# Kernel tuning notes

Hardware: AMD Instinct MI355X
Metric: run time of the kernel (lower is better)

The kernel has to match this reference:

```python
import jax, jax.numpy as jnp
import numpy as np

B, S, D, H = 2, 2048, 768, 12
DK = D // H


def setup_inputs() -> dict:
    key = jax.random.key(0)
    ks = jax.random.split(key, 10)
    sc = 0.02
    return {
        "k": jax.random.normal(ks[0], (B, S, D), jnp.float32),
        "q": jax.random.normal(ks[1], (B, S, D), jnp.float32),
        "v": jax.random.normal(ks[2], (B, S, D), jnp.float32),
        "mask": jnp.ones((B, 1, S, S), jnp.int32),
        "wq": jax.random.normal(ks[3], (D, D), jnp.float32) * sc,
        "bq": jnp.zeros((D,), jnp.float32),
        "wk": jax.random.normal(ks[4], (D, D), jnp.float32) * sc,
        "bk": jnp.zeros((D,), jnp.float32),
        "wv": jax.random.normal(ks[5], (D, D), jnp.float32) * sc,
        "bv": jnp.zeros((D,), jnp.float32),
        "wo": jax.random.normal(ks[6], (D, D), jnp.float32) * sc,
        "bo": jnp.zeros((D,), jnp.float32),
    }


def reference(k, q, v, mask, wq, bq, wk, bk, wv, bv, wo, bo):
    # Linear projections (torch Linear: x @ W^T + b)
    query = q @ wq.T + bq
    key_ = k @ wk.T + bk
    value = v @ wv.T + bv
    # [B,S,D] -> [B,H,S,DK]
    def split_heads(x):
        return x.reshape(B, S, H, DK).transpose(0, 2, 1, 3)
    Q, K, V = split_heads(query), split_heads(key_), split_heads(value)
    # NOTE: original masked_fill result is discarded -> mask is a no-op.
    scores = jnp.einsum("bhqd,bhkd->bhqk", Q, K) / jnp.sqrt(jnp.float32(DK))
    attn = jax.nn.softmax(scores, axis=-1)  # dropout p=0.0 -> identity
    out = jnp.einsum("bhqk,bhkd->bhqd", attn, V)
    out = out.transpose(0, 2, 1, 3).reshape(B, S, D)
    return out @ wo.T + bo
```

## Files before the change

### kernel.cpp

```cpp
#include <hip/hip_runtime.h>
#include <hip/hip_bf16.h>

#define B_  2
#define S_  2048
#define D_  768
#define H_  12
#define DK_ 64
#define NX_ (B_*S_*D_)
#define NW_ (D_*D_)
#define CSC 0.18033688011112042f

typedef __attribute__((ext_vector_type(8))) short  bf16x8;
typedef __attribute__((ext_vector_type(4))) float  f32x4;

__device__ __forceinline__ unsigned short f2bf(float f) {
    unsigned int u = __float_as_uint(f);
    u += 0x7fffu + ((u >> 16) & 1u);
    return (unsigned short)(u >> 16);
}

__device__ __forceinline__ unsigned pack_bf2(float a, float b) {
    const unsigned ua = __float_as_uint(a) + 0x8000u;
    const unsigned ub = __float_as_uint(b) + 0x8000u;
    return __builtin_amdgcn_perm(ub, ua, 0x07060302u);
}

__device__ __forceinline__ void async_cp16(const unsigned short* g,
                                           const unsigned short* lds_uniform_base) {
    __builtin_amdgcn_global_load_lds(
        (const __attribute__((address_space(1))) unsigned int*)(uintptr_t)g,
        (__attribute__((address_space(3))) unsigned int*)(unsigned int)(uintptr_t)lds_uniform_base,
        16, 0, 0);
}

struct CvtArgs { const float* s[7]; };

__global__ __launch_bounds__(256) void cvt_all(CvtArgs a,
                                               unsigned short* __restrict__ Xsw,
                                               unsigned short* __restrict__ Wsw) {
    const int bx = blockIdx.x;
    int y, inner;
    if (bx < 4608) { y = bx / 1536;       inner = bx % 1536; }
    else           { y = 3 + (bx - 4608) / 288; inner = (bx - 4608) % 288; }
    const int idx = inner * 256 + threadIdx.x;
    const int n = idx / 96;
    const int g = idx % 96;
    const float* src = a.s[y];
    const float zs = (y == 3) ? CSC : 1.0f;
    const float4 f0 = *(const float4*)(src + (long)n * D_ + g * 8);
    const float4 f1 = *(const float4*)(src + (long)n * D_ + g * 8 + 4);
    unsigned short o[8] = {f2bf(f0.x*zs), f2bf(f0.y*zs), f2bf(f0.z*zs), f2bf(f0.w*zs),
                           f2bf(f1.x*zs), f2bf(f1.y*zs), f2bf(f1.z*zs), f2bf(f1.w*zs)};
    const int kdst = (g >> 3) * 64 + (((g & 7) ^ (n & 7)) * 8);
    unsigned short* dst = (y >= 3) ? (Wsw + (long)(y - 3) * NW_) : (Xsw + (long)y * NX_);
    *(uint4*)(dst + (long)n * D_ + kdst) = *(const uint4*)o;
}

struct QkvArgs { const float* bias[3]; unsigned short* out[3]; };

__global__ __launch_bounds__(256, 2) void gemm_qkv(QkvArgs args,
                                                   const unsigned short* __restrict__ Xsw,
                                                   const unsigned short* __restrict__ Wsw) {
    __shared__ __align__(16) unsigned short smem[17408];
    unsigned short* As = smem;
    unsigned short* Bs = smem + 8192;

    const int t    = threadIdx.x;
    const int wave = t >> 6;
    const int lane = t & 63;
    const int l16  = lane & 15;
    const int quad = lane >> 4;
    const int wm   = wave >> 1, wn = wave & 1;
    const int m0   = blockIdx.x * 128;
    const int zz   = blockIdx.y / 6;
    const int nb   = blockIdx.y % 6;
    const int n0   = nb * 128;

    const unsigned short* Ap = Xsw + (long)zz * NX_;
    const unsigned short* Wp = Wsw + (long)zz * NW_;

    f32x4 acc[4][4];
#pragma unroll
    for (int s = 0; s < 4; s++)
#pragma unroll
        for (int j = 0; j < 4; j++) acc[s][j] = (f32x4){0.f, 0.f, 0.f, 0.f};

    const int lrow = lane >> 3;
    const int lcg  = lane & 7;

    for (int k0 = 0; k0 < D_; k0 += 64) {
        __syncthreads();
#pragma unroll
        for (int i = 0; i < 4; i++) {
            const int chunk = wave * 4 + i;
            async_cp16(Ap + (long)(m0 + chunk * 8 + lrow) * D_ + k0 + lcg * 8,
                       As + chunk * 512);
        }
#pragma unroll
        for (int i = 0; i < 4; i++) {
            const int chunk = wave * 4 + i;
            async_cp16(Wp + (long)(n0 + chunk * 8 + lrow) * D_ + k0 + lcg * 8,
                       Bs + chunk * 512);
        }
        __syncthreads();
#pragma unroll
        for (int ks = 0; ks < 2; ks++) {
            const int cg = ks * 4 + quad;
            bf16x8 af[4], bf[4];
#pragma unroll
            for (int s = 0; s < 4; s++) {
                const int r = wm * 64 + s * 16 + l16;
                af[s] = *(const bf16x8*)&As[r * 64 + ((cg ^ (r & 7)) * 8)];
            }
#pragma unroll
            for (int j = 0; j < 4; j++) {
                const int r = wn * 64 + j * 16 + l16;
                bf[j] = *(const bf16x8*)&Bs[r * 64 + ((cg ^ (r & 7)) * 8)];
            }
#pragma unroll
            for (int s = 0; s < 4; s++)
#pragma unroll
                for (int j = 0; j < 4; j++)
                    acc[s][j] = __builtin_amdgcn_mfma_f32_16x16x32_bf16(af[s], bf[j], acc[s][j], 0, 0, 0);
        }
    }
    __syncthreads();

    const int b     = m0 >> 11;
    const int sbase = m0 & (S_ - 1);
    const float zs  = (zz == 0) ? CSC : 1.0f;
    float bv[4];
#pragma unroll
    for (int j = 0; j < 4; j++) bv[j] = args.bias[zz][n0 + wn * 64 + j * 16 + l16] * zs;

    if (zz < 2) {
        unsigned short* Ls = smem;
#pragma unroll
        for (int s = 0; s < 4; s++)
#pragma unroll
            for (int j = 0; j < 4; j++)
#pragma unroll
                for (int r = 0; r < 4; r++)
                    Ls[(wm * 64 + s * 16 + quad * 4 + r) * 136 + wn * 64 + j * 16 + l16] =
                        f2bf(acc[s][j][r] + bv[j]);
        __syncthreads();
        const int row  = t >> 1;
        const int half = t & 1;
        unsigned short* Op = args.out[zz];
#pragma unroll
        for (int i = 0; i < 8; i++) {
            const int col  = half * 64 + i * 8;
            const int head = nb * 2 + half;
            const uint4 v = *(const uint4*)&Ls[row * 136 + col];
            *(uint4*)(Op + ((long)(b * H_ + head) * S_ + sbase + row) * DK_ + (col & 63)) = v;
        }
    } else {
        unsigned short* Ls = smem;
#pragma unroll
        for (int s = 0; s < 4; s++)
#pragma unroll
            for (int j = 0; j < 4; j++)
#pragma unroll
                for (int r = 0; r < 4; r++) {
                    const int dk  = j * 16 + l16;
                    const int pos = wm * 64 + (quad * 4 + r) * 4 + s;
                    Ls[wn * 8704 + dk * 136 + pos] = f2bf(acc[s][j][r] + bv[j]);
                }
        __syncthreads();
        const int rowIdx = t >> 1;
        const int hh = rowIdx >> 6, dk = rowIdx & 63;
        const int half = t & 1;
        unsigned short* Op = args.out[2];
#pragma unroll
        for (int i = 0; i < 8; i++) {
            const int col = half * 64 + i * 8;
            const uint4 v = *(const uint4*)&Ls[hh * 8704 + dk * 136 + col];
            const int head = nb * 2 + hh;
            *(uint4*)(Op + ((long)(b * H_ + head) * DK_ + dk) * S_ + sbase + col) = v;
        }
    }
}

__global__ __launch_bounds__(256, 3) void attn_kernel(
    const unsigned short* __restrict__ Q, const unsigned short* __restrict__ K,
    const unsigned short* __restrict__ Vt, unsigned short* __restrict__ Ao)
{
    const int t    = threadIdx.x;
    const int wave = t >> 6;
    const int lane = t & 63;
    const int l16  = lane & 15;
    const int quad = lane >> 4;
    const int qtile = blockIdx.x;
    const int bh    = blockIdx.y;

    const unsigned short* Qp = Q  + (long)bh * S_ * DK_;
    const unsigned short* Kp = K  + (long)bh * S_ * DK_;
    const unsigned short* Vp = Vt + (long)bh * DK_ * S_;

    __shared__ __align__(16) unsigned short smem[23040];

    bf16x8 qfrag[2];
    {
        const long qoff = (long)(qtile * 64 + wave * 16 + l16) * DK_ + quad * 8;
        qfrag[0] = *(const bf16x8*)(Qp + qoff);
        qfrag[1] = *(const bf16x8*)(Qp + qoff + 32);
    }
    unsigned short* Ps = smem + 18432;

    const int srow = t >> 2;
    const int scg  = (t & 3) * 16;
    uint4 kreg[2], vreg[2];
    {
        const unsigned short* gk = Kp + (long)srow * DK_ + scg;
        const unsigned short* gv = Vp + (long)srow * S_ + scg;
        kreg[0] = *(const uint4*)gk;  kreg[1] = *(const uint4*)(gk + 8);
        vreg[0] = *(const uint4*)gv;  vreg[1] = *(const uint4*)(gv + 8);
    }
    *(uint4*)&smem[srow * 72 + scg]            = kreg[0];
    *(uint4*)&smem[srow * 72 + scg + 8]        = kreg[1];
    *(uint4*)&smem[9216 + srow * 72 + scg]     = vreg[0];
    *(uint4*)&smem[9216 + srow * 72 + scg + 8] = vreg[1];

    f32x4 oacc[4];
#pragma unroll
    for (int j = 0; j < 4; j++) oacc[j] = (f32x4){0.f, 0.f, 0.f, 0.f};
    float lsum[4] = {0.f, 0.f, 0.f, 0.f};

    for (int it = 0; it < 32; ++it) {
        const int co = (it & 1) * 4608;
        const int no = ((it & 1) ^ 1) * 4608;
        __syncthreads();
        const unsigned short* Ks = smem + co;
        const unsigned short* Vs = smem + 9216 + co;

        if (it < 31) {
            const int kv0 = (it + 1) * 64;
            const unsigned short* gk = Kp + (long)(kv0 + srow) * DK_ + scg;
            const unsigned short* gv = Vp + (long)srow * S_ + kv0 + scg;
            kreg[0] = *(const uint4*)gk;  kreg[1] = *(const uint4*)(gk + 8);
            vreg[0] = *(const uint4*)gv;  vreg[1] = *(const uint4*)(gv + 8);
        }

        f32x4 sacc[4];
#pragma unroll
        for (int j = 0; j < 4; j++) sacc[j] = (f32x4){0.f, 0.f, 0.f, 0.f};
#pragma unroll
        for (int ks = 0; ks < 2; ks++)
#pragma unroll
            for (int j = 0; j < 4; j++) {
                const bf16x8 bf = *(const bf16x8*)&Ks[(j * 16 + l16) * 72 + ks * 32 + quad * 8];
                sacc[j] = __builtin_amdgcn_mfma_f32_16x16x32_bf16(qfrag[ks], bf, sacc[j], 0, 0, 0);
            }

#pragma unroll
        for (int r = 0; r < 4; r++) {
            const float p0 = exp2f(sacc[0][r]);
            const float p1 = exp2f(sacc[1][r]);
            const float p2 = exp2f(sacc[2][r]);
            const float p3 = exp2f(sacc[3][r]);
            lsum[r] += (p0 + p1) + (p2 + p3);
            uint2 pk = {pack_bf2(p0, p1), pack_bf2(p2, p3)};
            *(uint2*)&Ps[(wave * 16 + quad * 4 + r) * 72 + l16 * 4] = pk;
        }

#pragma unroll
        for (int ks = 0; ks < 2; ks++) {
            const bf16x8 pf = *(const bf16x8*)&Ps[(wave * 16 + l16) * 72 + ks * 32 + quad * 8];
#pragma unroll
            for (int j = 0; j < 4; j++) {
                const bf16x8 vf = *(const bf16x8*)&Vs[(j * 16 + l16) * 72 + ks * 32 + quad * 8];
                oacc[j] = __builtin_amdgcn_mfma_f32_16x16x32_bf16(pf, vf, oacc[j], 0, 0, 0);
            }
        }

        if (it < 31) {
            *(uint4*)&smem[no + srow * 72 + scg]            = kreg[0];
            *(uint4*)&smem[no + srow * 72 + scg + 8]        = kreg[1];
            *(uint4*)&smem[9216 + no + srow * 72 + scg]     = vreg[0];
            *(uint4*)&smem[9216 + no + srow * 72 + scg + 8] = vreg[1];
        }
    }

#pragma unroll
    for (int r = 0; r < 4; r++) {
#pragma unroll
        for (int off = 1; off < 16; off <<= 1)
            lsum[r] += __shfl_xor(lsum[r], off, 64);
        lsum[r] = 1.f / lsum[r];
    }

    __syncthreads();
#pragma unroll
    for (int j = 0; j < 4; j++)
#pragma unroll
        for (int r = 0; r < 4; r++)
            Ps[(wave * 16 + quad * 4 + r) * 72 + j * 16 + l16] =
                f2bf(oacc[j][r] * lsum[r]);

    const int b = bh / H_, h = bh % H_;
    const int row = t >> 2;
    const int c0  = (t & 3) * 16;
    const int qrow = qtile * 64 + row;
    const int key  = qrow & 7;
    const uint4 v0 = *(const uint4*)&Ps[row * 72 + c0];
    const uint4 v1 = *(const uint4*)&Ps[row * 72 + c0 + 8];
    const int g8 = c0 >> 3;
    unsigned short* dst = Ao + (long)(b * S_ + qrow) * D_ + h * DK_;
    *(uint4*)(dst + ((g8 ^ key) * 8))       = v0;
    *(uint4*)(dst + (((g8 + 1) ^ key) * 8)) = v1;
}

__global__ __launch_bounds__(256, 2) void gemm_out(
    const unsigned short* __restrict__ A, const unsigned short* __restrict__ Wsw,
    const float* __restrict__ bias, float* __restrict__ Out)
{
    __shared__ __align__(16) unsigned short smem[17408];
    unsigned short* As = smem;
    unsigned short* Bs = smem + 8192;

    const int t    = threadIdx.x;
    const int wave = t >> 6;
    const int lane = t & 63;
    const int l16  = lane & 15;
    const int quad = lane >> 4;
    const int wm   = wave >> 1, wn = wave & 1;
    const int m0   = blockIdx.x * 128;
    const int n0   = blockIdx.y * 128;

    f32x4 acc[4][4];
#pragma unroll
    for (int s = 0; s < 4; s++)
#pragma unroll
        for (int j = 0; j < 4; j++) acc[s][j] = (f32x4){0.f, 0.f, 0.f, 0.f};

    const int lrow = lane >> 3;
    const int lcg  = lane & 7;

    for (int k0 = 0; k0 < D_; k0 += 64) {
        __syncthreads();
#pragma unroll
        for (int i = 0; i < 4; i++) {
            const int chunk = wave * 4 + i;
            async_cp16(A + (long)(m0 + chunk * 8 + lrow) * D_ + k0 + lcg * 8,
                       As + chunk * 512);
        }
#pragma unroll
        for (int i = 0; i < 4; i++) {
            const int chunk = wave * 4 + i;
            async_cp16(Wsw + (long)(n0 + chunk * 8 + lrow) * D_ + k0 + lcg * 8,
                       Bs + chunk * 512);
        }
        __syncthreads();
#pragma unroll
        for (int ks = 0; ks < 2; ks++) {
            const int cg = ks * 4 + quad;
            bf16x8 af[4], bf[4];
#pragma unroll
            for (int s = 0; s < 4; s++) {
                const int r = wm * 64 + s * 16 + l16;
                af[s] = *(const bf16x8*)&As[r * 64 + ((cg ^ (r & 7)) * 8)];
            }
#pragma unroll
            for (int j = 0; j < 4; j++) {
                const int r = wn * 64 + j * 16 + l16;
                bf[j] = *(const bf16x8*)&Bs[r * 64 + ((cg ^ (r & 7)) * 8)];
            }
#pragma unroll
            for (int s = 0; s < 4; s++)
#pragma unroll
                for (int j = 0; j < 4; j++)
                    acc[s][j] = __builtin_amdgcn_mfma_f32_16x16x32_bf16(af[s], bf[j], acc[s][j], 0, 0, 0);
        }
    }

    float bv[4];
#pragma unroll
    for (int j = 0; j < 4; j++) bv[j] = bias[n0 + wn * 64 + j * 16 + l16];

    float* fl = (float*)smem;
#pragma unroll
    for (int h = 0; h < 2; h++) {
        __syncthreads();
        if (wn == h) {
#pragma unroll
            for (int s = 0; s < 4; s++)
#pragma unroll
                for (int j = 0; j < 4; j++)
#pragma unroll
                    for (int r = 0; r < 4; r++)
                        fl[(wm * 64 + s * 16 + quad * 4 + r) * 67 + j * 16 + l16] =
                            acc[s][j][r] + bv[j];
        }
        __syncthreads();
        const int row = t >> 1, c0 = (t & 1) * 32;
#pragma unroll
        for (int i = 0; i < 8; i++) {
            const float4 v = *(const float4*)&fl[row * 67 + c0 + i * 4];
            *(float4*)(Out + (long)(m0 + row) * D_ + n0 + h * 64 + c0 + i * 4) = v;
        }
    }
}

extern "C" void kernel_launch(void* const* d_in, const int* in_sizes, int n_in,
                              void* d_out, int out_size, void* d_ws, size_t ws_size,
                              hipStream_t stream) {
    const float* k_in = (const float*)d_in[0];
    const float* q_in = (const float*)d_in[1];
    const float* v_in = (const float*)d_in[2];
    const float* wq = (const float*)d_in[4];
    const float* bq = (const float*)d_in[5];
    const float* wk = (const float*)d_in[6];
    const float* bk = (const float*)d_in[7];
    const float* wv = (const float*)d_in[8];
    const float* bv = (const float*)d_in[9];
    const float* wo = (const float*)d_in[10];
    const float* bo = (const float*)d_in[11];

    unsigned short* ws = (unsigned short*)d_ws;
    unsigned short* Wsw = ws;
    unsigned short* Qb  = Wsw + 4ll * NW_;
    unsigned short* Kb  = Qb + (long)NX_;
    unsigned short* Vt  = Kb + (long)NX_;
    unsigned short* Xsw = Vt + (long)NX_;
    unsigned short* Ao  = Xsw;

    CvtArgs ca;
    ca.s[0] = q_in; ca.s[1] = k_in; ca.s[2] = v_in;
    ca.s[3] = wq;   ca.s[4] = wk;   ca.s[5] = wv;  ca.s[6] = wo;
    cvt_all<<<dim3(5760), 256, 0, stream>>>(ca, Xsw, Wsw);

    QkvArgs qa;
    qa.bias[0] = bq; qa.bias[1] = bk; qa.bias[2] = bv;
    qa.out[0] = Qb;  qa.out[1] = Kb;  qa.out[2] = Vt;
    gemm_qkv<<<dim3(32, 18), 256, 0, stream>>>(qa, Xsw, Wsw);

    attn_kernel<<<dim3(S_ / 64, B_ * H_), 256, 0, stream>>>(Qb, Kb, Vt, Ao);

    gemm_out<<<dim3(32, 6), 256, 0, stream>>>(Ao, Wsw + 3ll * NW_, bo, (float*)d_out);
}
```

Baseline: 219.0 us.

## Halve attention block to two waves with two query subtiles; shrink output GEMM tiles

```diff
diff --git a/kernel.cpp b/kernel.cpp
--- a/kernel.cpp
+++ b/kernel.cpp
@@ -181,7 +181,7 @@
     }
 }
 
-__global__ __launch_bounds__(256, 3) void attn_kernel(
+__global__ __launch_bounds__(128, 2) void attn_kernel(
     const unsigned short* __restrict__ Q, const unsigned short* __restrict__ K,
     const unsigned short* __restrict__ Vt, unsigned short* __restrict__ Ao)
 {
@@ -198,33 +198,38 @@
     const unsigned short* Vp = Vt + (long)bh * DK_ * S_;
 
     __shared__ __align__(16) unsigned short smem[23040];
-
-    bf16x8 qfrag[2];
+    unsigned short* Ps = smem + 18432;
+
+    bf16x8 qfrag[2][2];
+#pragma unroll
+    for (int st = 0; st < 2; st++) {
+        const long qoff = (long)(qtile * 64 + wave * 32 + st * 16 + l16) * DK_ + quad * 8;
+        qfrag[st][0] = *(const bf16x8*)(Qp + qoff);
+        qfrag[st][1] = *(const bf16x8*)(Qp + qoff + 32);
+    }
+
+    const int srow = t >> 1;
+    const int sc0  = (t & 1) * 32;
+    uint4 kreg[4], vreg[4];
     {
-        const long qoff = (long)(qtile * 64 + wave * 16 + l16) * DK_ + quad * 8;
-        qfrag[0] = *(const bf16x8*)(Qp + qoff);
-        qfrag[1] = *(const bf16x8*)(Qp + qoff + 32);
-    }
-    unsigned short* Ps = smem + 18432;
-
-    const int srow = t >> 2;
-    const int scg  = (t & 3) * 16;
-    uint4 kreg[2], vreg[2];
-    {
-        const unsigned short* gk = Kp + (long)srow * DK_ + scg;
-        const unsigned short* gv = Vp + (long)srow * S_ + scg;
-        kreg[0] = *(const uint4*)gk;  kreg[1] = *(const uint4*)(gk + 8);
-        vreg[0] = *(const uint4*)gv;  vreg[1] = *(const uint4*)(gv + 8);
-    }
-    *(uint4*)&smem[srow * 72 + scg]            = kreg[0];
-    *(uint4*)&smem[srow * 72 + scg + 8]        = kreg[1];
-    *(uint4*)&smem[9216 + srow * 72 + scg]     = vreg[0];
-    *(uint4*)&smem[9216 + srow * 72 + scg + 8] = vreg[1];
-
-    f32x4 oacc[4];
-#pragma unroll
-    for (int j = 0; j < 4; j++) oacc[j] = (f32x4){0.f, 0.f, 0.f, 0.f};
-    float lsum[4] = {0.f, 0.f, 0.f, 0.f};
+        const unsigned short* gk = Kp + (long)srow * DK_ + sc0;
+        const unsigned short* gv = Vp + (long)srow * S_ + sc0;
+#pragma unroll
+        for (int i = 0; i < 4; i++) { kreg[i] = *(const uint4*)(gk + i * 8);
+                                      vreg[i] = *(const uint4*)(gv + i * 8); }
+    }
+#pragma unroll
+    for (int i = 0; i < 4; i++) {
+        *(uint4*)&smem[srow * 72 + sc0 + i * 8]        = kreg[i];
+        *(uint4*)&smem[9216 + srow * 72 + sc0 + i * 8] = vreg[i];
+    }
+
+    f32x4 oacc[2][4];
+#pragma unroll
+    for (int st = 0; st < 2; st++)
+#pragma unroll
+        for (int j = 0; j < 4; j++) oacc[st][j] = (f32x4){0.f, 0.f, 0.f, 0.f};
+    float lsum[2][4] = {{0.f,0.f,0.f,0.f},{0.f,0.f,0.f,0.f}};
 
     for (int it = 0; it < 32; ++it) {
         const int co = (it & 1) * 4608;
@@ -235,88 +240,107 @@
 
         if (it < 31) {
             const int kv0 = (it + 1) * 64;
-            const unsigned short* gk = Kp + (long)(kv0 + srow) * DK_ + scg;
-            const unsigned short* gv = Vp + (long)srow * S_ + kv0 + scg;
-            kreg[0] = *(const uint4*)gk;  kreg[1] = *(const uint4*)(gk + 8);
-            vreg[0] = *(const uint4*)gv;  vreg[1] = *(const uint4*)(gv + 8);
-        }
-
-        f32x4 sacc[4];
-#pragma unroll
-        for (int j = 0; j < 4; j++) sacc[j] = (f32x4){0.f, 0.f, 0.f, 0.f};
+            const unsigned short* gk = Kp + (long)(kv0 + srow) * DK_ + sc0;
+            const unsigned short* gv = Vp + (long)srow * S_ + kv0 + sc0;
+#pragma unroll
+            for (int i = 0; i < 4; i++) { kreg[i] = *(const uint4*)(gk + i * 8);
+                                          vreg[i] = *(const uint4*)(gv + i * 8); }
+        }
+
+        f32x4 sacc[2][4];
+#pragma unroll
+        for (int st = 0; st < 2; st++)
+#pragma unroll
+            for (int j = 0; j < 4; j++) sacc[st][j] = (f32x4){0.f, 0.f, 0.f, 0.f};
 #pragma unroll
         for (int ks = 0; ks < 2; ks++)
 #pragma unroll
             for (int j = 0; j < 4; j++) {
                 const bf16x8 bf = *(const bf16x8*)&Ks[(j * 16 + l16) * 72 + ks * 32 + quad * 8];
-                sacc[j] = __builtin_amdgcn_mfma_f32_16x16x32_bf16(qfrag[ks], bf, sacc[j], 0, 0, 0);
-            }
-
-#pragma unroll
-        for (int r = 0; r < 4; r++) {
-            const float p0 = exp2f(sacc[0][r]);
-            const float p1 = exp2f(sacc[1][r]);
-            const float p2 = exp2f(sacc[2][r]);
-            const float p3 = exp2f(sacc[3][r]);
-            lsum[r] += (p0 + p1) + (p2 + p3);
-            uint2 pk = {pack_bf2(p0, p1), pack_bf2(p2, p3)};
-            *(uint2*)&Ps[(wave * 16 + quad * 4 + r) * 72 + l16 * 4] = pk;
-        }
+#pragma unroll
+                for (int st = 0; st < 2; st++)
+                    sacc[st][j] = __builtin_amdgcn_mfma_f32_16x16x32_bf16(qfrag[st][ks], bf, sacc[st][j], 0, 0, 0);
+            }
+
+#pragma unroll
+        for (int st = 0; st < 2; st++)
+#pragma unroll
+            for (int r = 0; r < 4; r++) {
+                const float p0 = exp2f(sacc[st][0][r]);
+                const float p1 = exp2f(sacc[st][1][r]);
+                const float p2 = exp2f(sacc[st][2][r]);
+                const float p3 = exp2f(sacc[st][3][r]);
+                lsum[st][r] += (p0 + p1) + (p2 + p3);
+                uint2 pk = {pack_bf2(p0, p1), pack_bf2(p2, p3)};
+                *(uint2*)&Ps[(wave * 32 + st * 16 + quad * 4 + r) * 72 + l16 * 4] = pk;
+            }
 
 #pragma unroll
         for (int ks = 0; ks < 2; ks++) {
-            const bf16x8 pf = *(const bf16x8*)&Ps[(wave * 16 + l16) * 72 + ks * 32 + quad * 8];
+            bf16x8 pf[2];
+#pragma unroll
+            for (int st = 0; st < 2; st++)
+                pf[st] = *(const bf16x8*)&Ps[(wave * 32 + st * 16 + l16) * 72 + ks * 32 + quad * 8];
 #pragma unroll
             for (int j = 0; j < 4; j++) {
                 const bf16x8 vf = *(const bf16x8*)&Vs[(j * 16 + l16) * 72 + ks * 32 + quad * 8];
-                oacc[j] = __builtin_amdgcn_mfma_f32_16x16x32_bf16(pf, vf, oacc[j], 0, 0, 0);
+#pragma unroll
+                for (int st = 0; st < 2; st++)
+                    oacc[st][j] = __builtin_amdgcn_mfma_f32_16x16x32_bf16(pf[st], vf, oacc[st][j], 0, 0, 0);
             }
         }
 
         if (it < 31) {
-            *(uint4*)&smem[no + srow * 72 + scg]            = kreg[0];
-            *(uint4*)&smem[no + srow * 72 + scg + 8]        = kreg[1];
-            *(uint4*)&smem[9216 + no + srow * 72 + scg]     = vreg[0];
-            *(uint4*)&smem[9216 + no + srow * 72 + scg + 8] = vreg[1];
-        }
-    }
-
-#pragma unroll
-    for (int r = 0; r < 4; r++) {
-#pragma unroll
-        for (int off = 1; off < 16; off <<= 1)
-            lsum[r] += __shfl_xor(lsum[r], off, 64);
-        lsum[r] = 1.f / lsum[r];
-    }
+#pragma unroll
+            for (int i = 0; i < 4; i++) {
+                *(uint4*)&smem[no + srow * 72 + sc0 + i * 8]        = kreg[i];
+                *(uint4*)&smem[9216 + no + srow * 72 + sc0 + i * 8] = vreg[i];
+            }
+        }
+    }
+
+#pragma unroll
+    for (int st = 0; st < 2; st++)
+#pragma unroll
+        for (int r = 0; r < 4; r++) {
+#pragma unroll
+            for (int off = 1; off < 16; off <<= 1)
+                lsum[st][r] += __shfl_xor(lsum[st][r], off, 64);
+            lsum[st][r] = 1.f / lsum[st][r];
+        }
 
     __syncthreads();
 #pragma unroll
-    for (int j = 0; j < 4; j++)
-#pragma unroll
-        for (int r = 0; r < 4; r++)
-            Ps[(wave * 16 + quad * 4 + r) * 72 + j * 16 + l16] =
-                f2bf(oacc[j][r] * lsum[r]);
+    for (int st = 0; st < 2; st++)
+#pragma unroll
+        for (int j = 0; j < 4; j++)
+#pragma unroll
+            for (int r = 0; r < 4; r++)
+                Ps[(wave * 32 + st * 16 + quad * 4 + r) * 72 + j * 16 + l16] =
+                    f2bf(oacc[st][j][r] * lsum[st][r]);
+    __syncthreads();
 
     const int b = bh / H_, h = bh % H_;
-    const int row = t >> 2;
-    const int c0  = (t & 3) * 16;
+    const int row = t >> 1;
+    const int c0  = (t & 1) * 32;
     const int qrow = qtile * 64 + row;
     const int key  = qrow & 7;
-    const uint4 v0 = *(const uint4*)&Ps[row * 72 + c0];
-    const uint4 v1 = *(const uint4*)&Ps[row * 72 + c0 + 8];
-    const int g8 = c0 >> 3;
     unsigned short* dst = Ao + (long)(b * S_ + qrow) * D_ + h * DK_;
-    *(uint4*)(dst + ((g8 ^ key) * 8))       = v0;
-    *(uint4*)(dst + (((g8 + 1) ^ key) * 8)) = v1;
+#pragma unroll
+    for (int i = 0; i < 4; i++) {
+        const int g8 = (c0 >> 3) + i;
+        const uint4 v = *(const uint4*)&Ps[row * 72 + c0 + i * 8];
+        *(uint4*)(dst + ((g8 ^ key) * 8)) = v;
+    }
 }
 
 __global__ __launch_bounds__(256, 2) void gemm_out(
     const unsigned short* __restrict__ A, const unsigned short* __restrict__ Wsw,
     const float* __restrict__ bias, float* __restrict__ Out)
 {
-    __shared__ __align__(16) unsigned short smem[17408];
+    __shared__ __align__(16) unsigned short smem[8704];
     unsigned short* As = smem;
-    unsigned short* Bs = smem + 8192;
+    unsigned short* Bs = smem + 4096;
 
     const int t    = threadIdx.x;
     const int wave = t >> 6;
@@ -324,14 +348,14 @@
     const int l16  = lane & 15;
     const int quad = lane >> 4;
     const int wm   = wave >> 1, wn = wave & 1;
-    const int m0   = blockIdx.x * 128;
-    const int n0   = blockIdx.y * 128;
-
-    f32x4 acc[4][4];
-#pragma unroll
-    for (int s = 0; s < 4; s++)
-#pragma unroll
-        for (int j = 0; j < 4; j++) acc[s][j] = (f32x4){0.f, 0.f, 0.f, 0.f};
+    const int m0   = blockIdx.x * 64;
+    const int n0   = blockIdx.y * 64;
+
+    f32x4 acc[2][2];
+#pragma unroll
+    for (int s = 0; s < 2; s++)
+#pragma unroll
+        for (int j = 0; j < 2; j++) acc[s][j] = (f32x4){0.f, 0.f, 0.f, 0.f};
 
     const int lrow = lane >> 3;
     const int lcg  = lane & 7;
@@ -339,14 +363,14 @@
     for (int k0 = 0; k0 < D_; k0 += 64) {
         __syncthreads();
 #pragma unroll
-        for (int i = 0; i < 4; i++) {
-            const int chunk = wave * 4 + i;
+        for (int i = 0; i < 2; i++) {
+            const int chunk = wave * 2 + i;
             async_cp16(A + (long)(m0 + chunk * 8 + lrow) * D_ + k0 + lcg * 8,
                        As + chunk * 512);
         }
 #pragma unroll
-        for (int i = 0; i < 4; i++) {
-            const int chunk = wave * 4 + i;
+        for (int i = 0; i < 2; i++) {
+            const int chunk = wave * 2 + i;
             async_cp16(Wsw + (long)(n0 + chunk * 8 + lrow) * D_ + k0 + lcg * 8,
                        Bs + chunk * 512);
         }
@@ -354,50 +378,45 @@
 #pragma unroll
         for (int ks = 0; ks < 2; ks++) {
             const int cg = ks * 4 + quad;
-            bf16x8 af[4], bf[4];
-#pragma unroll
-            for (int s = 0; s < 4; s++) {
-                const int r = wm * 64 + s * 16 + l16;
+            bf16x8 af[2], bf[2];
+#pragma unroll
+            for (int s = 0; s < 2; s++) {
+                const int r = wm * 32 + s * 16 + l16;
                 af[s] = *(const bf16x8*)&As[r * 64 + ((cg ^ (r & 7)) * 8)];
             }
 #pragma unroll
-            for (int j = 0; j < 4; j++) {
-                const int r = wn * 64 + j * 16 + l16;
+            for (int j = 0; j < 2; j++) {
+                const int r = wn * 32 + j * 16 + l16;
                 bf[j] = *(const bf16x8*)&Bs[r * 64 + ((cg ^ (r & 7)) * 8)];
             }
 #pragma unroll
-            for (int s = 0; s < 4; s++)
-#pragma unroll
-                for (int j = 0; j < 4; j++)
+            for (int s = 0; s < 2; s++)
+#pragma unroll
+                for (int j = 0; j < 2; j++)
                     acc[s][j] = __builtin_amdgcn_mfma_f32_16x16x32_bf16(af[s], bf[j], acc[s][j], 0, 0, 0);
         }
     }
 
-    float bv[4];
-#pragma unroll
-    for (int j = 0; j < 4; j++) bv[j] = bias[n0 + wn * 64 + j * 16 + l16];
-
+    float bv[2];
+#pragma unroll
+    for (int j = 0; j < 2; j++) bv[j] = bias[n0 + wn * 32 + j * 16 + l16];
+
+    __syncthreads();
     float* fl = (float*)smem;
 #pragma unroll
-    for (int h = 0; h < 2; h++) {
-        __syncthreads();
-        if (wn == h) {
-#pragma unroll
-            for (int s = 0; s < 4; s++)
-#pragma unroll
-                for (int j = 0; j < 4; j++)
-#pragma unroll
-                    for (int r = 0; r < 4; r++)
-                        fl[(wm * 64 + s * 16 + quad * 4 + r) * 67 + j * 16 + l16] =
-                            acc[s][j][r] + bv[j];
-        }
-        __syncthreads();
-        const int row = t >> 1, c0 = (t & 1) * 32;
-#pragma unroll
-        for (int i = 0; i < 8; i++) {
-            const float4 v = *(const float4*)&fl[row * 67 + c0 + i * 4];
-            *(float4*)(Out + (long)(m0 + row) * D_ + n0 + h * 64 + c0 + i * 4) = v;
-        }
+    for (int s = 0; s < 2; s++)
+#pragma unroll
+        for (int j = 0; j < 2; j++)
+#pragma unroll
+            for (int r = 0; r < 4; r++)
+                fl[(wm * 32 + s * 16 + quad * 4 + r) * 67 + wn * 32 + j * 16 + l16] =
+                    acc[s][j][r] + bv[j];
+    __syncthreads();
+    const int row = t >> 2, c0 = (t & 3) * 16;
+#pragma unroll
+    for (int i = 0; i < 4; i++) {
+        const float4 v = *(const float4*)&fl[row * 67 + c0 + i * 4];
+        *(float4*)(Out + (long)(m0 + row) * D_ + n0 + c0 + i * 4) = v;
     }
 }
 
@@ -434,7 +453,7 @@
     qa.out[0] = Qb;  qa.out[1] = Kb;  qa.out[2] = Vt;
     gemm_qkv<<<dim3(32, 18), 256, 0, stream>>>(qa, Xsw, Wsw);
 
-    attn_kernel<<<dim3(S_ / 64, B_ * H_), 256, 0, stream>>>(Qb, Kb, Vt, Ao);
-
-    gemm_out<<<dim3(32, 6), 256, 0, stream>>>(Ao, Wsw + 3ll * NW_, bo, (float*)d_out);
-}
+    attn_kernel<<<dim3(S_ / 64, B_ * H_), 128, 0, stream>>>(Qb, Kb, Vt, Ao);
+
+    gemm_out<<<dim3(64, 12), 256, 0, stream>>>(Ao, Wsw + 3ll * NW_, bo, (float*)d_out);
+}
```

Result: slower. 223.7 us (+2.1%).

## Shrink output GEMM tiles to 64x64, unroll attention loop by two, raise occupancy

Applied to the files above, without the earlier changes.

```diff
diff --git a/kernel.cpp b/kernel.cpp
--- a/kernel.cpp
+++ b/kernel.cpp
@@ -58,7 +58,7 @@
 
 struct QkvArgs { const float* bias[3]; unsigned short* out[3]; };
 
-__global__ __launch_bounds__(256, 2) void gemm_qkv(QkvArgs args,
+__global__ __launch_bounds__(256, 3) void gemm_qkv(QkvArgs args,
                                                    const unsigned short* __restrict__ Xsw,
                                                    const unsigned short* __restrict__ Wsw) {
     __shared__ __align__(16) unsigned short smem[17408];
@@ -198,6 +198,7 @@
     const unsigned short* Vp = Vt + (long)bh * DK_ * S_;
 
     __shared__ __align__(16) unsigned short smem[23040];
+    unsigned short* Ps = smem + 18432;
 
     bf16x8 qfrag[2];
     {
@@ -205,81 +206,84 @@
         qfrag[0] = *(const bf16x8*)(Qp + qoff);
         qfrag[1] = *(const bf16x8*)(Qp + qoff + 32);
     }
-    unsigned short* Ps = smem + 18432;
 
     const int srow = t >> 2;
     const int scg  = (t & 3) * 16;
     uint4 kreg[2], vreg[2];
     {
-        const unsigned short* gk = Kp + (long)srow * DK_ + scg;
-        const unsigned short* gv = Vp + (long)srow * S_ + scg;
-        kreg[0] = *(const uint4*)gk;  kreg[1] = *(const uint4*)(gk + 8);
-        vreg[0] = *(const uint4*)gv;  vreg[1] = *(const uint4*)(gv + 8);
+        const unsigned short* gk0 = Kp + (long)srow * DK_ + scg;
+        const unsigned short* gv0 = Vp + (long)srow * S_ + scg;
+        kreg[0] = *(const uint4*)gk0;  kreg[1] = *(const uint4*)(gk0 + 8);
+        vreg[0] = *(const uint4*)gv0;  vreg[1] = *(const uint4*)(gv0 + 8);
     }
     *(uint4*)&smem[srow * 72 + scg]            = kreg[0];
     *(uint4*)&smem[srow * 72 + scg + 8]        = kreg[1];
     *(uint4*)&smem[9216 + srow * 72 + scg]     = vreg[0];
     *(uint4*)&smem[9216 + srow * 72 + scg + 8] = vreg[1];
 
+    const unsigned short* gk = Kp + (long)(64 + srow) * DK_ + scg;
+    const unsigned short* gv = Vp + (long)srow * S_ + 64 + scg;
+
     f32x4 oacc[4];
 #pragma unroll
     for (int j = 0; j < 4; j++) oacc[j] = (f32x4){0.f, 0.f, 0.f, 0.f};
     float lsum[4] = {0.f, 0.f, 0.f, 0.f};
 
-    for (int it = 0; it < 32; ++it) {
-        const int co = (it & 1) * 4608;
-        const int no = ((it & 1) ^ 1) * 4608;
-        __syncthreads();
-        const unsigned short* Ks = smem + co;
-        const unsigned short* Vs = smem + 9216 + co;
-
-        if (it < 31) {
-            const int kv0 = (it + 1) * 64;
-            const unsigned short* gk = Kp + (long)(kv0 + srow) * DK_ + scg;
-            const unsigned short* gv = Vp + (long)srow * S_ + kv0 + scg;
-            kreg[0] = *(const uint4*)gk;  kreg[1] = *(const uint4*)(gk + 8);
-            vreg[0] = *(const uint4*)gv;  vreg[1] = *(const uint4*)(gv + 8);
-        }
-
-        f32x4 sacc[4];
-#pragma unroll
-        for (int j = 0; j < 4; j++) sacc[j] = (f32x4){0.f, 0.f, 0.f, 0.f};
-#pragma unroll
-        for (int ks = 0; ks < 2; ks++)
-#pragma unroll
-            for (int j = 0; j < 4; j++) {
-                const bf16x8 bf = *(const bf16x8*)&Ks[(j * 16 + l16) * 72 + ks * 32 + quad * 8];
-                sacc[j] = __builtin_amdgcn_mfma_f32_16x16x32_bf16(qfrag[ks], bf, sacc[j], 0, 0, 0);
-            }
-
-#pragma unroll
-        for (int r = 0; r < 4; r++) {
-            const float p0 = exp2f(sacc[0][r]);
-            const float p1 = exp2f(sacc[1][r]);
-            const float p2 = exp2f(sacc[2][r]);
-            const float p3 = exp2f(sacc[3][r]);
-            lsum[r] += (p0 + p1) + (p2 + p3);
-            uint2 pk = {pack_bf2(p0, p1), pack_bf2(p2, p3)};
-            *(uint2*)&Ps[(wave * 16 + quad * 4 + r) * 72 + l16 * 4] = pk;
-        }
-
-#pragma unroll
-        for (int ks = 0; ks < 2; ks++) {
-            const bf16x8 pf = *(const bf16x8*)&Ps[(wave * 16 + l16) * 72 + ks * 32 + quad * 8];
-#pragma unroll
-            for (int j = 0; j < 4; j++) {
-                const bf16x8 vf = *(const bf16x8*)&Vs[(j * 16 + l16) * 72 + ks * 32 + quad * 8];
-                oacc[j] = __builtin_amdgcn_mfma_f32_16x16x32_bf16(pf, vf, oacc[j], 0, 0, 0);
-            }
-        }
-
-        if (it < 31) {
-            *(uint4*)&smem[no + srow * 72 + scg]            = kreg[0];
-            *(uint4*)&smem[no + srow * 72 + scg + 8]        = kreg[1];
-            *(uint4*)&smem[9216 + no + srow * 72 + scg]     = vreg[0];
-            *(uint4*)&smem[9216 + no + srow * 72 + scg + 8] = vreg[1];
-        }
-    }
+#define ATTN_STEP(CO, NO, PF)                                                  \
+    {                                                                          \
+        __syncthreads();                                                       \
+        if (PF) {                                                              \
+            kreg[0] = *(const uint4*)gk;  kreg[1] = *(const uint4*)(gk + 8);   \
+            vreg[0] = *(const uint4*)gv;  vreg[1] = *(const uint4*)(gv + 8);   \
+            gk += 64 * DK_;  gv += 64;                                         \
+        }                                                                      \
+        f32x4 sacc[4];                                                         \
+        _Pragma("unroll")                                                      \
+        for (int j = 0; j < 4; j++) sacc[j] = (f32x4){0.f, 0.f, 0.f, 0.f};     \
+        _Pragma("unroll")                                                      \
+        for (int ks = 0; ks < 2; ks++)                                         \
+            _Pragma("unroll")                                                  \
+            for (int j = 0; j < 4; j++) {                                      \
+                const bf16x8 bf = *(const bf16x8*)&smem[(CO) +                 \
+                    (j * 16 + l16) * 72 + ks * 32 + quad * 8];                 \
+                sacc[j] = __builtin_amdgcn_mfma_f32_16x16x32_bf16(             \
+                    qfrag[ks], bf, sacc[j], 0, 0, 0);                          \
+            }                                                                  \
+        _Pragma("unroll")                                                      \
+        for (int r = 0; r < 4; r++) {                                          \
+            const float p0 = exp2f(sacc[0][r]);                                \
+            const float p1 = exp2f(sacc[1][r]);                                \
+            const float p2 = exp2f(sacc[2][r]);                                \
+            const float p3 = exp2f(sacc[3][r]);                                \
+            lsum[r] += (p0 + p1) + (p2 + p3);                                  \
+            uint2 pk = {pack_bf2(p0, p1), pack_bf2(p2, p3)};                   \
+            *(uint2*)&Ps[(wave * 16 + quad * 4 + r) * 72 + l16 * 4] = pk;      \
+        }                                                                      \
+        _Pragma("unroll")                                                      \
+        for (int ks = 0; ks < 2; ks++) {                                       \
+            const bf16x8 pf = *(const bf16x8*)&Ps[(wave * 16 + l16) * 72 +     \
+                ks * 32 + quad * 8];                                           \
+            _Pragma("unroll")                                                  \
+            for (int j = 0; j < 4; j++) {                                      \
+                const bf16x8 vf = *(const bf16x8*)&smem[9216 + (CO) +          \
+                    (j * 16 + l16) * 72 + ks * 32 + quad * 8];                 \
+                oacc[j] = __builtin_amdgcn_mfma_f32_16x16x32_bf16(             \
+                    pf, vf, oacc[j], 0, 0, 0);                                 \
+            }                                                                  \
+        }                                                                      \
+        if (PF) {                                                              \
+            *(uint4*)&smem[(NO) + srow * 72 + scg]            = kreg[0];       \
+            *(uint4*)&smem[(NO) + srow * 72 + scg + 8]        = kreg[1];       \
+            *(uint4*)&smem[9216 + (NO) + srow * 72 + scg]     = vreg[0];       \
+            *(uint4*)&smem[9216 + (NO) + srow * 72 + scg + 8] = vreg[1];       \
+        }                                                                      \
+    }
+
+    for (int it2 = 0; it2 < 16; ++it2) {
+        ATTN_STEP(0, 4608, 1)
+        ATTN_STEP(4608, 0, (it2 < 15))
+    }
+#undef ATTN_STEP
 
 #pragma unroll
     for (int r = 0; r < 4; r++) {
@@ -310,13 +314,13 @@
     *(uint4*)(dst + (((g8 + 1) ^ key) * 8)) = v1;
 }
 
-__global__ __launch_bounds__(256, 2) void gemm_out(
+__global__ __launch_bounds__(256, 4) void gemm_out(
     const unsigned short* __restrict__ A, const unsigned short* __restrict__ Wsw,
     const float* __restrict__ bias, float* __restrict__ Out)
 {
-    __shared__ __align__(16) unsigned short smem[17408];
+    __shared__ __align__(16) unsigned short smem[8704];
     unsigned short* As = smem;
-    unsigned short* Bs = smem + 8192;
+    unsigned short* Bs = smem + 4096;
 
     const int t    = threadIdx.x;
     const int wave = t >> 6;
@@ -324,14 +328,14 @@
     const int l16  = lane & 15;
     const int quad = lane >> 4;
     const int wm   = wave >> 1, wn = wave & 1;
-    const int m0   = blockIdx.x * 128;
-    const int n0   = blockIdx.y * 128;
-
-    f32x4 acc[4][4];
-#pragma unroll
-    for (int s = 0; s < 4; s++)
-#pragma unroll
-        for (int j = 0; j < 4; j++) acc[s][j] = (f32x4){0.f, 0.f, 0.f, 0.f};
+    const int m0   = blockIdx.x * 64;
+    const int n0   = blockIdx.y * 64;
+
+    f32x4 acc[2][2];
+#pragma unroll
+    for (int s = 0; s < 2; s++)
+#pragma unroll
+        for (int j = 0; j < 2; j++) acc[s][j] = (f32x4){0.f, 0.f, 0.f, 0.f};
 
     const int lrow = lane >> 3;
     const int lcg  = lane & 7;
@@ -339,14 +343,14 @@
     for (int k0 = 0; k0 < D_; k0 += 64) {
         __syncthreads();
 #pragma unroll
-        for (int i = 0; i < 4; i++) {
-            const int chunk = wave * 4 + i;
+        for (int i = 0; i < 2; i++) {
+            const int chunk = wave * 2 + i;
             async_cp16(A + (long)(m0 + chunk * 8 + lrow) * D_ + k0 + lcg * 8,
                        As + chunk * 512);
         }
 #pragma unroll
-        for (int i = 0; i < 4; i++) {
-            const int chunk = wave * 4 + i;
+        for (int i = 0; i < 2; i++) {
+            const int chunk = wave * 2 + i;
             async_cp16(Wsw + (long)(n0 + chunk * 8 + lrow) * D_ + k0 + lcg * 8,
                        Bs + chunk * 512);
         }
@@ -354,50 +358,45 @@
 #pragma unroll
         for (int ks = 0; ks < 2; ks++) {
             const int cg = ks * 4 + quad;
-            bf16x8 af[4], bf[4];
-#pragma unroll
-            for (int s = 0; s < 4; s++) {
-                const int r = wm * 64 + s * 16 + l16;
+            bf16x8 af[2], bf[2];
+#pragma unroll
+            for (int s = 0; s < 2; s++) {
+                const int r = wm * 32 + s * 16 + l16;
                 af[s] = *(const bf16x8*)&As[r * 64 + ((cg ^ (r & 7)) * 8)];
             }
 #pragma unroll
-            for (int j = 0; j < 4; j++) {
-                const int r = wn * 64 + j * 16 + l16;
+            for (int j = 0; j < 2; j++) {
+                const int r = wn * 32 + j * 16 + l16;
                 bf[j] = *(const bf16x8*)&Bs[r * 64 + ((cg ^ (r & 7)) * 8)];
             }
 #pragma unroll
-            for (int s = 0; s < 4; s++)
-#pragma unroll
-                for (int j = 0; j < 4; j++)
+            for (int s = 0; s < 2; s++)
+#pragma unroll
+                for (int j = 0; j < 2; j++)
                     acc[s][j] = __builtin_amdgcn_mfma_f32_16x16x32_bf16(af[s], bf[j], acc[s][j], 0, 0, 0);
         }
     }
 
-    float bv[4];
-#pragma unroll
-    for (int j = 0; j < 4; j++) bv[j] = bias[n0 + wn * 64 + j * 16 + l16];
-
+    float bv[2];
+#pragma unroll
+    for (int j = 0; j < 2; j++) bv[j] = bias[n0 + wn * 32 + j * 16 + l16];
+
+    __syncthreads();
     float* fl = (float*)smem;
 #pragma unroll
-    for (int h = 0; h < 2; h++) {
-        __syncthreads();
-        if (wn == h) {
-#pragma unroll
-            for (int s = 0; s < 4; s++)
-#pragma unroll
-                for (int j = 0; j < 4; j++)
-#pragma unroll
-                    for (int r = 0; r < 4; r++)
-                        fl[(wm * 64 + s * 16 + quad * 4 + r) * 67 + j * 16 + l16] =
-                            acc[s][j][r] + bv[j];
-        }
-        __syncthreads();
-        const int row = t >> 1, c0 = (t & 1) * 32;
-#pragma unroll
-        for (int i = 0; i < 8; i++) {
-            const float4 v = *(const float4*)&fl[row * 67 + c0 + i * 4];
-            *(float4*)(Out + (long)(m0 + row) * D_ + n0 + h * 64 + c0 + i * 4) = v;
-        }
+    for (int s = 0; s < 2; s++)
+#pragma unroll
+        for (int j = 0; j < 2; j++)
+#pragma unroll
+            for (int r = 0; r < 4; r++)
+                fl[(wm * 32 + s * 16 + quad * 4 + r) * 67 + wn * 32 + j * 16 + l16] =
+                    acc[s][j][r] + bv[j];
+    __syncthreads();
+    const int row = t >> 2, c0 = (t & 3) * 16;
+#pragma unroll
+    for (int i = 0; i < 4; i++) {
+        const float4 v = *(const float4*)&fl[row * 67 + c0 + i * 4];
+        *(float4*)(Out + (long)(m0 + row) * D_ + n0 + c0 + i * 4) = v;
     }
 }
 
@@ -436,5 +435,5 @@
 
     attn_kernel<<<dim3(S_ / 64, B_ * H_), 256, 0, stream>>>(Qb, Kb, Vt, Ao);
 
-    gemm_out<<<dim3(32, 6), 256, 0, stream>>>(Ao, Wsw + 3ll * NW_, bo, (float*)d_out);
-}
+    gemm_out<<<dim3(64, 12), 256, 0, stream>>>(Ao, Wsw + 3ll * NW_, bo, (float*)d_out);
+}
```

Result: faster. 214.6 us (-2.0%).
